# Optimization experiments

Hardware: AMD Instinct MI355X
Metric: run time of the kernel (lower is better)

Reference implementation:

```python
import jax, jax.numpy as jnp
import numpy as np

H1, H, OUT, T = 512, 2048, 1024, 4096

def setup_inputs() -> dict:
    key = jax.random.key(0)
    ks = jax.random.split(key, 20)
    s = 0.02
    return {
        "input": jax.random.normal(ks[0], (1, OUT), jnp.float32),
        "hidden": jax.random.normal(ks[1], (1, 1, H), jnp.float32) * 0.1,
        "encoder_outputs": jax.random.normal(ks[2], (T, H), jnp.float32),
        "prenet_w": jax.random.normal(ks[3], (H1, OUT), jnp.float32) * s,
        "prenet_b": jnp.zeros((H1,), jnp.float32),
        "prenet2_w": jax.random.normal(ks[4], (H, H1), jnp.float32) * s,
        "prenet2_b": jnp.zeros((H,), jnp.float32),
        "attn1_w": jax.random.normal(ks[5], (H, H), jnp.float32) * s,
        "attn2_w": jax.random.normal(ks[6], (H, H), jnp.float32) * s,
        "attn3_w": jax.random.normal(ks[7], (1, H), jnp.float32) * s,
        "gru_w_ih": jax.random.normal(ks[8], (3 * H, 2 * H), jnp.float32) * s,
        "gru_w_hh": jax.random.normal(ks[9], (3 * H, H), jnp.float32) * s,
        "gru_b_ih": jnp.zeros((3 * H,), jnp.float32),
        "gru_b_hh": jnp.zeros((3 * H,), jnp.float32),
        "lin_w": jax.random.normal(ks[10], (OUT, H), jnp.float32) * s,
        "lin_b": jnp.zeros((OUT,), jnp.float32),
    }

def reference(input, hidden, encoder_outputs, prenet_w, prenet_b, prenet2_w,
              prenet2_b, attn1_w, attn2_w, attn3_w, gru_w_ih, gru_w_hh,
              gru_b_ih, gru_b_hh, lin_w, lin_b):
    # prenet MLP (dropout in eval mode = identity)
    em6 = jax.nn.relu(jax.nn.relu(input @ prenet_w.T + prenet_b) @ prenet2_w.T + prenet2_b)  # [1,H]
    # Bahdanau additive attention
    way = em6 @ attn1_w.T                                 # [1,H]
    uah = encoder_outputs @ attn2_w.T                     # [T,H]
    beta = jnp.tanh(way + uah)                            # [T,H] (broadcast = expand_as)
    gamma = beta @ attn3_w.T                              # [T,1]
    attn_weights = jax.nn.softmax(gamma.T, axis=1)        # [1,T]
    attn_applied = attn_weights @ encoder_outputs         # [1,H]
    # single-step GRU (PyTorch gate order: r, z, n)
    x = jnp.concatenate([em6, attn_applied], axis=1)      # [1,2H]
    h0 = hidden[0]                                        # [1,H]
    gi = x @ gru_w_ih.T + gru_b_ih                        # [1,3H]
    gh = h0 @ gru_w_hh.T + gru_b_hh                       # [1,3H]
    i_r, i_z, i_n = jnp.split(gi, 3, axis=1)
    h_r, h_z, h_n = jnp.split(gh, 3, axis=1)
    r = jax.nn.sigmoid(i_r + h_r)
    z = jax.nn.sigmoid(i_z + h_z)
    n = jnp.tanh(i_n + r * h_n)
    h_new = (1.0 - z) * n + z * h0                        # [1,H]
    out = jax.nn.softmax(h_new @ lin_w.T + lin_b, axis=1) # [1,OUT]
    return out, h_new[None], attn_weights
```

## Files before the change

kernel.cpp:

```cpp
#include <hip/hip_runtime.h>
#include <hip/hip_bf16.h>

typedef __bf16 bf16x8 __attribute__((ext_vector_type(8)));
typedef __bf16 bf16x4 __attribute__((ext_vector_type(4)));
typedef float f32x4 __attribute__((ext_vector_type(4)));

#define H1 512
#define H 2048
#define OUTN 1024
#define T 4096

__global__ __launch_bounds__(256) void matvec_k(
    const float* __restrict__ W, const float* __restrict__ x,
    const float* __restrict__ b, float* __restrict__ out,
    int R, int K, int relu)
{
    int row = blockIdx.x * 4 + (threadIdx.x >> 6);
    int lane = threadIdx.x & 63;
    if (row >= R) return;
    const float* Wr = W + (size_t)row * K;
    float s = 0.f;
    for (int k = lane * 4; k < K; k += 256) {
        float4 w4 = *(const float4*)(Wr + k);
        float4 x4 = *(const float4*)(x + k);
        s += w4.x * x4.x + w4.y * x4.y + w4.z * x4.z + w4.w * x4.w;
    }
    #pragma unroll
    for (int m = 32; m; m >>= 1) s += __shfl_xor(s, m, 64);
    if (lane == 0) {
        if (b) s += b[row];
        if (relu) s = fmaxf(s, 0.f);
        out[row] = s;
    }
}

__global__ __launch_bounds__(256) void cvt_sw_k(
    const float* __restrict__ E, const float* __restrict__ W2,
    __bf16* __restrict__ dst)
{
    int c = blockIdx.x * 256 + threadIdx.x;
    int row = c >> 8;
    int kc = c & 255;
    const float* src = (row < T) ? (E + (size_t)row * H + kc * 8)
                                 : (W2 + (size_t)(row - T) * H + kc * 8);
    float4 a = *(const float4*)src;
    float4 b = *(const float4*)(src + 4);
    bf16x8 v = {(__bf16)a.x, (__bf16)a.y, (__bf16)a.z, (__bf16)a.w,
                (__bf16)b.x, (__bf16)b.y, (__bf16)b.z, (__bf16)b.w};
    int grp = kc >> 3, cc = kc & 7;
    int sw = cc ^ (row & 7);
    *(bf16x8*)(dst + (size_t)row * H + grp * 64 + sw * 8) = v;
}

__global__ __launch_bounds__(256) void gamma_gemm2(
    const __bf16* __restrict__ Asw,
    const __bf16* __restrict__ Bsw,
    const float* __restrict__ way, const float* __restrict__ a3,
    float* __restrict__ gamma)
{
    __shared__ __attribute__((aligned(16))) __bf16 As[128][64];
    __shared__ __attribute__((aligned(16))) __bf16 Bs[128][64];
    __shared__ float wayS[128], a3S[128];

    const int tb = blockIdx.x, hb = blockIdx.y;
    const int tid = threadIdx.x, lane = tid & 63, wid = tid >> 6;
    const int wr = wid >> 1, wc = wid & 1;
    if (tid < 128) { wayS[tid] = way[hb * 128 + tid]; a3S[tid] = a3[hb * 128 + tid]; }

    const int K = 2048;
    const __bf16* Ap = Asw + (size_t)(tb * 128) * K;
    const __bf16* Bp = Bsw + (size_t)(hb * 128) * K;

    f32x4 acc[4][4] = {};
    const int rl = lane & 15;
    const int kg = (lane >> 4) * 8;

    const int c0 = wid * 256;
    for (int k0 = 0; k0 < K; k0 += 64) {
        __syncthreads();
        #pragma unroll
        for (int j = 0; j < 4; ++j) {
            int c = c0 + j * 64 + lane;
            int row = c >> 3, cc = c & 7;
            const __bf16* sA = Ap + (size_t)row * K + k0 + cc * 8;
            const __bf16* sB = Bp + (size_t)row * K + k0 + cc * 8;
            __builtin_amdgcn_global_load_lds(
                (const __attribute__((address_space(1))) void*)sA,
                (__attribute__((address_space(3))) void*)((char*)&As[0][0] + (c0 + j * 64) * 16),
                16, 0, 0);
            __builtin_amdgcn_global_load_lds(
                (const __attribute__((address_space(1))) void*)sB,
                (__attribute__((address_space(3))) void*)((char*)&Bs[0][0] + (c0 + j * 64) * 16),
                16, 0, 0);
        }
        __syncthreads();
        #pragma unroll
        for (int kk = 0; kk < 2; ++kk) {
            bf16x8 af[4], bfm[4];
            const int kb = (kg + kk * 32) * 2;
            #pragma unroll
            for (int mi = 0; mi < 4; ++mi) {
                int r = wr * 64 + mi * 16 + rl;
                af[mi] = *(const bf16x8*)((const char*)&As[0][0] + r * 128 + (kb ^ ((r & 7) << 4)));
            }
            #pragma unroll
            for (int ni = 0; ni < 4; ++ni) {
                int r = wc * 64 + ni * 16 + rl;
                bfm[ni] = *(const bf16x8*)((const char*)&Bs[0][0] + r * 128 + (kb ^ ((r & 7) << 4)));
            }
            #pragma unroll
            for (int mi = 0; mi < 4; ++mi)
                #pragma unroll
                for (int ni = 0; ni < 4; ++ni)
                    acc[mi][ni] = __builtin_amdgcn_mfma_f32_16x16x32_bf16(
                        af[mi], bfm[ni], acc[mi][ni], 0, 0, 0);
        }
    }

    const int rg = lane >> 4;
    #pragma unroll
    for (int mi = 0; mi < 4; ++mi) {
        float sr[4] = {0.f, 0.f, 0.f, 0.f};
        #pragma unroll
        for (int ni = 0; ni < 4; ++ni) {
            int h = wc * 64 + ni * 16 + rl;
            float wh = wayS[h];
            float ah = a3S[h];
            #pragma unroll
            for (int r = 0; r < 4; ++r)
                sr[r] += tanhf(wh + acc[mi][ni][r]) * ah;
        }
        #pragma unroll
        for (int m = 1; m < 16; m <<= 1) {
            #pragma unroll
            for (int r = 0; r < 4; ++r)
                sr[r] += __shfl_xor(sr[r], m, 64);
        }
        if (rl == 0) {
            int t = tb * 128 + wr * 64 + mi * 16 + rg * 4;
            #pragma unroll
            for (int r = 0; r < 4; ++r)
                atomicAdd(&gamma[t + r], sr[r]);
        }
    }
}

#define BM 128
#define BN 128
#define BK 32
#define LSTR 40

__global__ __launch_bounds__(256) void gamma_gemm(
    const float* __restrict__ E, const float* __restrict__ W2,
    const float* __restrict__ way, const float* __restrict__ a3,
    float* __restrict__ gamma)
{
    __shared__ __bf16 As[BM][LSTR];
    __shared__ __bf16 Bs[BN][LSTR];
    __shared__ float wayS[BN];
    __shared__ float a3S[BN];

    const int tb = blockIdx.x, hb = blockIdx.y;
    const int tid = threadIdx.x, lane = tid & 63, wid = tid >> 6;
    const int wr = wid >> 1, wc = wid & 1;
    if (tid < BN) { wayS[tid] = way[hb * BN + tid]; a3S[tid] = a3[hb * BN + tid]; }

    f32x4 acc[4][4] = {};
    const int K = 2048;
    const float* Ep  = E  + (size_t)(tb * BM) * K;
    const float* W2p = W2 + (size_t)(hb * BN) * K;
    const int rl = lane & 15;
    const int kg = (lane >> 4) * 8;

    for (int k0 = 0; k0 < K; k0 += BK) {
        __syncthreads();
        #pragma unroll
        for (int i = 0; i < 4; ++i) {
            int c = tid + i * 256;
            int row = c >> 3;
            int col = (c & 7) * 4;
            float4 va = *(const float4*)(Ep + (size_t)row * K + k0 + col);
            bf16x4 pa = {(__bf16)va.x, (__bf16)va.y, (__bf16)va.z, (__bf16)va.w};
            *(bf16x4*)&As[row][col] = pa;
            float4 vb = *(const float4*)(W2p + (size_t)row * K + k0 + col);
            bf16x4 pb = {(__bf16)vb.x, (__bf16)vb.y, (__bf16)vb.z, (__bf16)vb.w};
            *(bf16x4*)&Bs[row][col] = pb;
        }
        __syncthreads();
        bf16x8 af[4], bfr[4];
        #pragma unroll
        for (int mi = 0; mi < 4; ++mi)
            af[mi] = *(const bf16x8*)&As[wr * 64 + mi * 16 + rl][kg];
        #pragma unroll
        for (int ni = 0; ni < 4; ++ni)
            bfr[ni] = *(const bf16x8*)&Bs[wc * 64 + ni * 16 + rl][kg];
        #pragma unroll
        for (int mi = 0; mi < 4; ++mi)
            #pragma unroll
            for (int ni = 0; ni < 4; ++ni)
                acc[mi][ni] = __builtin_amdgcn_mfma_f32_16x16x32_bf16(
                    af[mi], bfr[ni], acc[mi][ni], 0, 0, 0);
    }

    const int rg = lane >> 4;
    #pragma unroll
    for (int mi = 0; mi < 4; ++mi) {
        float sr[4] = {0.f, 0.f, 0.f, 0.f};
        #pragma unroll
        for (int ni = 0; ni < 4; ++ni) {
            int h = wc * 64 + ni * 16 + rl;
            float wh = wayS[h];
            float ah = a3S[h];
            #pragma unroll
            for (int r = 0; r < 4; ++r)
                sr[r] += tanhf(wh + acc[mi][ni][r]) * ah;
        }
        #pragma unroll
        for (int m = 1; m < 16; m <<= 1) {
            #pragma unroll
            for (int r = 0; r < 4; ++r)
                sr[r] += __shfl_xor(sr[r], m, 64);
        }
        if (rl == 0) {
            int t = tb * BM + wr * 64 + mi * 16 + rg * 4;
            #pragma unroll
            for (int r = 0; r < 4; ++r)
                atomicAdd(&gamma[t + r], sr[r]);
        }
    }
}

__global__ __launch_bounds__(1024) void softmax_k(
    const float* __restrict__ in, float* __restrict__ out, int n)
{
    __shared__ float sred[16];
    __shared__ float sbc;
    int tid = threadIdx.x;

    float m = -3.4e38f;
    for (int i = tid; i < n; i += 1024) m = fmaxf(m, in[i]);
    #pragma unroll
    for (int s = 32; s; s >>= 1) m = fmaxf(m, __shfl_xor(m, s, 64));
    if ((tid & 63) == 0) sred[tid >> 6] = m;
    __syncthreads();
    if (tid == 0) {
        float mm = sred[0];
        for (int i = 1; i < 16; ++i) mm = fmaxf(mm, sred[i]);
        sbc = mm;
    }
    __syncthreads();
    float mx = sbc;

    float s = 0.f;
    for (int i = tid; i < n; i += 1024) s += expf(in[i] - mx);
    #pragma unroll
    for (int sh = 32; sh; sh >>= 1) s += __shfl_xor(s, sh, 64);
    if ((tid & 63) == 0) sred[tid >> 6] = s;
    __syncthreads();
    if (tid == 0) {
        float ss = 0.f;
        for (int i = 0; i < 16; ++i) ss += sred[i];
        sbc = ss;
    }
    __syncthreads();
    float inv = 1.f / sbc;
    for (int i = tid; i < n; i += 1024) out[i] = expf(in[i] - mx) * inv;
}

__global__ __launch_bounds__(256) void attn_apply_k(
    const float* __restrict__ E, const float* __restrict__ w,
    float* __restrict__ outacc)
{
    int tid = threadIdx.x;
    int t0 = blockIdx.x * 32;
    float a[8] = {0.f, 0.f, 0.f, 0.f, 0.f, 0.f, 0.f, 0.f};
    for (int t = t0; t < t0 + 32; ++t) {
        float wt = w[t];
        const float* Er = E + (size_t)t * H;
        #pragma unroll
        for (int j = 0; j < 8; ++j)
            a[j] += wt * Er[tid + 256 * j];
    }
    #pragma unroll
    for (int j = 0; j < 8; ++j)
        atomicAdd(&outacc[tid + 256 * j], a[j]);
}

__global__ __launch_bounds__(256) void gru_combine_k(
    const float* __restrict__ gi, const float* __restrict__ gh,
    const float* __restrict__ h0, float* __restrict__ hout)
{
    int h = blockIdx.x * 256 + threadIdx.x;
    float ir = gi[h], iz = gi[H + h], in_ = gi[2 * H + h];
    float hr = gh[h], hz = gh[H + h], hn = gh[2 * H + h];
    float r = 1.f / (1.f + expf(-(ir + hr)));
    float z = 1.f / (1.f + expf(-(iz + hz)));
    float n = tanhf(in_ + r * hn);
    hout[h] = (1.f - z) * n + z * h0[h];
}

extern "C" void kernel_launch(void* const* d_in, const int* in_sizes, int n_in,
                              void* d_out, int out_size, void* d_ws, size_t ws_size,
                              hipStream_t stream)
{
    const float* input    = (const float*)d_in[0];
    const float* hidden   = (const float*)d_in[1];
    const float* enc      = (const float*)d_in[2];
    const float* prenet_w = (const float*)d_in[3];
    const float* prenet_b = (const float*)d_in[4];
    const float* prenet2_w= (const float*)d_in[5];
    const float* prenet2_b= (const float*)d_in[6];
    const float* attn1_w  = (const float*)d_in[7];
    const float* attn2_w  = (const float*)d_in[8];
    const float* attn3_w  = (const float*)d_in[9];
    const float* gru_w_ih = (const float*)d_in[10];
    const float* gru_w_hh = (const float*)d_in[11];
    const float* gru_b_ih = (const float*)d_in[12];
    const float* gru_b_hh = (const float*)d_in[13];
    const float* lin_w    = (const float*)d_in[14];
    const float* lin_b    = (const float*)d_in[15];

    float* out = (float*)d_out;
    float* h_new = out + OUTN;
    float* attn_w = out + OUTN + H;

    float* ws = (float*)d_ws;
    float* w_h1     = ws;
    float* w_way    = w_h1 + 512;
    float* w_gamma  = w_way + H;
    float* w_x      = w_gamma + T;
    float* w_gi     = w_x + 2 * H;
    float* w_gh     = w_gi + 3 * H;
    float* w_logits = w_gh + 3 * H;

    const size_t BF_OFF = 131072;
    const size_t BF_BYTES = (size_t)(T + H) * H * sizeof(__bf16);
    bool fast = (ws_size >= BF_OFF + BF_BYTES);
    __bf16* bfE  = (__bf16*)((char*)d_ws + BF_OFF);
    __bf16* bfW2 = bfE + (size_t)T * H;

    hipMemsetAsync(w_gamma, 0, T * sizeof(float), stream);
    hipMemsetAsync(w_x + H, 0, H * sizeof(float), stream);

    if (fast)
        cvt_sw_k<<<(T + H) * (H / 8) / 256, 256, 0, stream>>>(enc, attn2_w, bfE);

    matvec_k<<<H1 / 4, 256, 0, stream>>>(prenet_w, input, prenet_b, w_h1, H1, OUTN, 1);
    matvec_k<<<H / 4, 256, 0, stream>>>(prenet2_w, w_h1, prenet2_b, w_x, H, H1, 1);
    matvec_k<<<H / 4, 256, 0, stream>>>(attn1_w, w_x, nullptr, w_way, H, H, 0);

    if (fast)
        gamma_gemm2<<<dim3(T / 128, H / 128), 256, 0, stream>>>(bfE, bfW2, w_way, attn3_w, w_gamma);
    else
        gamma_gemm<<<dim3(T / BM, H / BN), 256, 0, stream>>>(enc, attn2_w, w_way, attn3_w, w_gamma);

    softmax_k<<<1, 1024, 0, stream>>>(w_gamma, attn_w, T);
    attn_apply_k<<<T / 32, 256, 0, stream>>>(enc, attn_w, w_x + H);
    matvec_k<<<(3 * H) / 4, 256, 0, stream>>>(gru_w_ih, w_x, gru_b_ih, w_gi, 3 * H, 2 * H, 0);
    matvec_k<<<(3 * H) / 4, 256, 0, stream>>>(gru_w_hh, hidden, gru_b_hh, w_gh, 3 * H, H, 0);
    gru_combine_k<<<H / 256, 256, 0, stream>>>(w_gi, w_gh, hidden, h_new);
    matvec_k<<<OUTN / 4, 256, 0, stream>>>(lin_w, h_new, lin_b, w_logits, OUTN, H, 0);
    softmax_k<<<1, 1024, 0, stream>>>(w_logits, out, OUTN);
}
```

Baseline: 129.1 us.

## Double-buffer LDS in bf16 gamma GEMM and enlarge tile to 256x128

Replaces the single-buffered gamma GEMM with a double-buffered version that issues global-to-LDS loads for the next K slice while MFMAs run on the current one. The block grows to 512 threads (8 waves) covering 256 T-rows by 128 H-columns, which halves the grid along T and reuses each B tile across more rows. The goal is to hide global load latency and cut redundant reads of W2. In exchange, LDS use per block roughly triples, which may lower occupancy, and the full vmcnt(0) wait each iteration limits how much overlap is possible.

Measured after the change: 132.2 us. 2.4% more time.

```diff
diff --git a/kernel.cpp b/kernel.cpp
--- a/kernel.cpp
+++ b/kernel.cpp
@@ -52,70 +52,95 @@
     *(bf16x8*)(dst + (size_t)row * H + grp * 64 + sw * 8) = v;
 }
 
-__global__ __launch_bounds__(256) void gamma_gemm2(
+__global__ __launch_bounds__(512) void gamma_gemm3(
     const __bf16* __restrict__ Asw,
     const __bf16* __restrict__ Bsw,
     const float* __restrict__ way, const float* __restrict__ a3,
     float* __restrict__ gamma)
 {
-    __shared__ __attribute__((aligned(16))) __bf16 As[128][64];
-    __shared__ __attribute__((aligned(16))) __bf16 Bs[128][64];
+    __shared__ __attribute__((aligned(16))) __bf16 As[2][256][64];
+    __shared__ __attribute__((aligned(16))) __bf16 Bs[2][128][64];
     __shared__ float wayS[128], a3S[128];
 
     const int tb = blockIdx.x, hb = blockIdx.y;
     const int tid = threadIdx.x, lane = tid & 63, wid = tid >> 6;
-    const int wr = wid >> 1, wc = wid & 1;
+    const int wr = wid >> 1;
+    const int wc = wid & 1;
     if (tid < 128) { wayS[tid] = way[hb * 128 + tid]; a3S[tid] = a3[hb * 128 + tid]; }
 
     const int K = 2048;
-    const __bf16* Ap = Asw + (size_t)(tb * 128) * K;
+    const __bf16* Ap = Asw + (size_t)(tb * 256) * K;
     const __bf16* Bp = Bsw + (size_t)(hb * 128) * K;
 
     f32x4 acc[4][4] = {};
     const int rl = lane & 15;
     const int kg = (lane >> 4) * 8;
 
-    const int c0 = wid * 256;
-    for (int k0 = 0; k0 < K; k0 += 64) {
+    #define STAGE(buf, k0)                                                      \
+    do {                                                                        \
+        _Pragma("unroll")                                                       \
+        for (int j = 0; j < 4; ++j) {                                           \
+            int c = tid + j * 512;                                              \
+            int row_ = c >> 3, cc_ = c & 7;                                     \
+            const __bf16* s_ = Ap + (size_t)row_ * K + (k0) + cc_ * 8;          \
+            __builtin_amdgcn_global_load_lds(                                   \
+                (const __attribute__((address_space(1))) void*)s_,              \
+                (__attribute__((address_space(3))) void*)((char*)&As[buf][0][0] + c * 16), \
+                16, 0, 0);                                                      \
+        }                                                                       \
+        _Pragma("unroll")                                                       \
+        for (int j = 0; j < 2; ++j) {                                           \
+            int c = tid + j * 512;                                              \
+            int row_ = c >> 3, cc_ = c & 7;                                     \
+            const __bf16* s_ = Bp + (size_t)row_ * K + (k0) + cc_ * 8;          \
+            __builtin_amdgcn_global_load_lds(                                   \
+                (const __attribute__((address_space(1))) void*)s_,              \
+                (__attribute__((address_space(3))) void*)((char*)&Bs[buf][0][0] + c * 16), \
+                16, 0, 0);                                                      \
+        }                                                                       \
+    } while (0)
+
+    #define COMPUTE(buf)                                                        \
+    do {                                                                        \
+        _Pragma("unroll")                                                       \
+        for (int kk = 0; kk < 2; ++kk) {                                        \
+            bf16x8 af[4], bfm[4];                                               \
+            const int kb = (kg + kk * 32) * 2;                                  \
+            _Pragma("unroll")                                                   \
+            for (int mi = 0; mi < 4; ++mi) {                                    \
+                int r_ = wr * 64 + mi * 16 + rl;                                \
+                af[mi] = *(const bf16x8*)((const char*)&As[buf][0][0] + r_ * 128 + (kb ^ ((r_ & 7) << 4))); \
+            }                                                                   \
+            _Pragma("unroll")                                                   \
+            for (int ni = 0; ni < 4; ++ni) {                                    \
+                int r_ = wc * 64 + ni * 16 + rl;                                \
+                bfm[ni] = *(const bf16x8*)((const char*)&Bs[buf][0][0] + r_ * 128 + (kb ^ ((r_ & 7) << 4))); \
+            }                                                                   \
+            _Pragma("unroll")                                                   \
+            for (int mi = 0; mi < 4; ++mi)                                      \
+                _Pragma("unroll")                                               \
+                for (int ni = 0; ni < 4; ++ni)                                  \
+                    acc[mi][ni] = __builtin_amdgcn_mfma_f32_16x16x32_bf16(      \
+                        af[mi], bfm[ni], acc[mi][ni], 0, 0, 0);                 \
+        }                                                                       \
+    } while (0)
+
+    STAGE(0, 0);
+    asm volatile("s_waitcnt vmcnt(0)" ::: "memory");
+    __syncthreads();
+
+    int cur = 0;
+    for (int t = 0; t < 31; ++t) {
+        STAGE(cur ^ 1, (t + 1) * 64);
+        COMPUTE(cur);
+        asm volatile("s_waitcnt vmcnt(0)" ::: "memory");
         __syncthreads();
-        #pragma unroll
-        for (int j = 0; j < 4; ++j) {
-            int c = c0 + j * 64 + lane;
-            int row = c >> 3, cc = c & 7;
-            const __bf16* sA = Ap + (size_t)row * K + k0 + cc * 8;
-            const __bf16* sB = Bp + (size_t)row * K + k0 + cc * 8;
-            __builtin_amdgcn_global_load_lds(
-                (const __attribute__((address_space(1))) void*)sA,
-                (__attribute__((address_space(3))) void*)((char*)&As[0][0] + (c0 + j * 64) * 16),
-                16, 0, 0);
-            __builtin_amdgcn_global_load_lds(
-                (const __attribute__((address_space(1))) void*)sB,
-                (__attribute__((address_space(3))) void*)((char*)&Bs[0][0] + (c0 + j * 64) * 16),
-                16, 0, 0);
-        }
-        __syncthreads();
-        #pragma unroll
-        for (int kk = 0; kk < 2; ++kk) {
-            bf16x8 af[4], bfm[4];
-            const int kb = (kg + kk * 32) * 2;
-            #pragma unroll
-            for (int mi = 0; mi < 4; ++mi) {
-                int r = wr * 64 + mi * 16 + rl;
-                af[mi] = *(const bf16x8*)((const char*)&As[0][0] + r * 128 + (kb ^ ((r & 7) << 4)));
-            }
-            #pragma unroll
-            for (int ni = 0; ni < 4; ++ni) {
-                int r = wc * 64 + ni * 16 + rl;
-                bfm[ni] = *(const bf16x8*)((const char*)&Bs[0][0] + r * 128 + (kb ^ ((r & 7) << 4)));
-            }
-            #pragma unroll
-            for (int mi = 0; mi < 4; ++mi)
-                #pragma unroll
-                for (int ni = 0; ni < 4; ++ni)
-                    acc[mi][ni] = __builtin_amdgcn_mfma_f32_16x16x32_bf16(
-                        af[mi], bfm[ni], acc[mi][ni], 0, 0, 0);
-        }
-    }
+        cur ^= 1;
+    }
+    COMPUTE(cur);
+
+    #undef STAGE
+    #undef COMPUTE
 
     const int rg = lane >> 4;
     #pragma unroll
@@ -137,7 +162,7 @@
                 sr[r] += __shfl_xor(sr[r], m, 64);
         }
         if (rl == 0) {
-            int t = tb * 128 + wr * 64 + mi * 16 + rg * 4;
+            int t = tb * 256 + wr * 64 + mi * 16 + rg * 4;
             #pragma unroll
             for (int r = 0; r < 4; ++r)
                 atomicAdd(&gamma[t + r], sr[r]);
@@ -350,7 +375,7 @@
     matvec_k<<<H / 4, 256, 0, stream>>>(attn1_w, w_x, nullptr, w_way, H, H, 0);
 
     if (fast)
-        gamma_gemm2<<<dim3(T / 128, H / 128), 256, 0, stream>>>(bfE, bfW2, w_way, attn3_w, w_gamma);
+        gamma_gemm3<<<dim3(T / 256, H / 128), 512, 0, stream>>>(bfE, bfW2, w_way, attn3_w, w_gamma);
     else
         gamma_gemm<<<dim3(T / BM, H / BN), 256, 0, stream>>>(enc, attn2_w, w_way, attn3_w, w_gamma);
 
```
